# Performance work log

Hardware: AMD Instinct MI355X
Metric: run time of the kernel (lower is better)

## Reference

```python
import jax, jax.numpy as jnp
import numpy as np

C_IN = 128   # pair channel dim
H = 4        # heads
DH = 32      # per-head dim (c_hidden // no_heads = 128 // 4)
R = 96       # low-rank bias rank (hard-coded self.Rank)
N = 384      # sequence length (pair rep is N x N)
S_DIM = 449  # s_inputs feature dim (c_in + 449 into bias MLPs)
MLP_H = 256  # bias MLP hidden width
EPS = 1e-5


def setup_inputs() -> dict:
    key = jax.random.key(0)
    ks = jax.random.split(key, 16)
    w = lambda k, shp, s=0.02: (jax.random.normal(k, shp) * s).astype(jnp.float32)
    return {
        "x": jax.random.normal(ks[0], (N, N, C_IN), dtype=jnp.float32),
        "s_inputs": jax.random.normal(ks[1], (N, S_DIM), dtype=jnp.float32),
        "ln_gamma": jnp.ones((C_IN,), jnp.float32),
        "ln_beta": jnp.zeros((C_IN,), jnp.float32),
        # q flashbias MLP (Linear->Tanh->Linear->Tanh->Linear, no bias)
        "Wq1": w(ks[2], (C_IN + S_DIM, MLP_H)),
        "Wq2": w(ks[3], (MLP_H, MLP_H)),
        "Wq3": w(ks[4], (MLP_H, H * R)),
        # k flashbias MLP
        "Wk1": w(ks[5], (C_IN + S_DIM, MLP_H)),
        "Wk2": w(ks[6], (MLP_H, MLP_H)),
        "Wk3": w(ks[7], (MLP_H, H * R)),
        # OpenFold-style gated Attention params
        "Wq_att": w(ks[8], (C_IN, H * DH)),
        "Wk_att": w(ks[9], (C_IN, H * DH)),
        "Wv_att": w(ks[10], (C_IN, H * DH)),
        "Wg": w(ks[11], (C_IN, H * DH)),
        "bg": jnp.zeros((H * DH,), jnp.float32),
        "Wo": w(ks[12], (H * DH, C_IN)),
        "bo": jnp.zeros((C_IN,), jnp.float32),
        "id": 10,  # id < 16 -> low-rank flashbias path
    }


def _layer_norm(x, gamma, beta):
    mu = jnp.mean(x, axis=-1, keepdims=True)
    var = jnp.var(x, axis=-1, keepdims=True)
    return (x - mu) * jax.lax.rsqrt(var + EPS) * gamma + beta


def _bias_mlp(z, W1, W2, W3):
    # [N, C+449] -> [N, H*R] -> [1, H, N, R]
    h = jnp.tanh(jnp.tanh(z @ W1) @ W2) @ W3
    return jnp.transpose(h.reshape(N, H, R), (1, 0, 2))[None]


def reference(x, s_inputs, ln_gamma, ln_beta, Wq1, Wq2, Wq3, Wk1, Wk2, Wk3,
              Wq_att, Wk_att, Wv_att, Wg, bg, Wo, bo, id=10):
    # starting=True, eval mode, s_inputs given, id < 16 -> low-rank bias path
    x = _layer_norm(x, ln_gamma, ln_beta)                       # [N, N, C]

    # low-rank triangle-bias factors (shared across rows, broadcast over dim 0)
    q_bias = _bias_mlp(jnp.concatenate([x.mean(1), s_inputs], -1), Wq1, Wq2, Wq3)  # [1,H,N,R]
    k_bias = _bias_mlp(jnp.concatenate([x.mean(0), s_inputs], -1), Wk1, Wk2, Wk3)  # [1,H,N,R]

    # multi-head attention over the last sequence axis, per row
    def heads(z, W):  # [N, N, C] -> [N, H, N, DH]
        return jnp.transpose((z @ W).reshape(N, N, H, DH), (0, 2, 1, 3))

    q = heads(x, Wq_att) * (1.0 / np.sqrt(DH)).astype(np.float32)
    k = heads(x, Wk_att)
    v = heads(x, Wv_att)

    scores = jnp.einsum("ihqd,ihkd->ihqk", q, k)                # [N,H,N,N]
    scores = scores + jnp.einsum("bhqr,bhkr->bhqk", q_bias, k_bias)  # broadcast over rows
    a = jax.nn.softmax(scores, axis=-1)

    o = jnp.einsum("ihqk,ihkd->ihqd", a, v)                     # [N,H,N,DH]
    o = jnp.transpose(o, (0, 2, 1, 3)).reshape(N, N, H * DH)
    g = jax.nn.sigmoid(x @ Wg + bg)                              # gating
    out = (g * o) @ Wo + bo                                      # [N, N, C]
    return out
```

## Files before the change

### kernel.cpp

```cpp
#include <hip/hip_runtime.h>
#include <cstdint>
#include <cstddef>

typedef _Float16 f16;
typedef __attribute__((ext_vector_type(2))) _Float16 f16x2;
typedef __attribute__((ext_vector_type(4))) _Float16 f16x4;
typedef __attribute__((ext_vector_type(8))) _Float16 f16x8;
typedef __attribute__((ext_vector_type(4))) float f32x4;

#define MFMA_16x16x32(a,b,c) __builtin_amdgcn_mfma_f32_16x16x32_f16((a),(b),(c),0,0,0)
#define MFMA_16x16x16(a,b,c) __builtin_amdgcn_mfma_f32_16x16x16f16((a),(b),(c),0,0,0)

#define NSEQ 384
#define CIN 128
#define NH 4
#define DHD 32
#define RNK 96
#define SDIM 449
#define MHID 256
#define NN (NSEQ*NSEQ)
#define LOG2E 1.4426950408889634f

#define KPAD 608
#define ZSTR 616
#define HSTR 264
#define OFF_W1 0
#define SZ_W1 (MHID*KPAD)
#define OFF_W2 (2*SZ_W1)
#define SZ_W2 (MHID*MHID)
#define OFF_W3 (OFF_W2 + 2*SZ_W2)
#define SZ_W3 ((NH*RNK)*MHID)
#define WMLP_TOT (OFF_W3 + 2*SZ_W3)

__global__ __launch_bounds__(256) void k_convert(const float* __restrict__ Wq, const float* __restrict__ Wk,
    const float* __restrict__ Wv, const float* __restrict__ Wg, const float* __restrict__ Wo,
    f16* __restrict__ W4T, f16* __restrict__ WoT) {
  int idx = blockIdx.x*256 + threadIdx.x;
  int c = idx >> 7, kk = idx & 127;
  if (c < 512) {
    int mat = c >> 7, cc = c & 127;
    const float* src = mat==0 ? Wq : (mat==1 ? Wk : (mat==2 ? Wv : Wg));
    W4T[c*CIN + kk] = (f16)src[kk*CIN + cc];
  } else {
    int cc = c - 512;
    WoT[cc*CIN + kk] = (f16)Wo[kk*CIN + cc];
  }
}

__global__ __launch_bounds__(256) void k_convert2(const float* __restrict__ Wq1, const float* __restrict__ Wq2,
    const float* __restrict__ Wq3, const float* __restrict__ Wk1, const float* __restrict__ Wk2,
    const float* __restrict__ Wk3, f16* __restrict__ wmlp) {
  int idx = blockIdx.x*256 + threadIdx.x;
  float val;
  if (idx < OFF_W2) {
    int m = idx / SZ_W1, r = idx - m*SZ_W1;
    int c = r / KPAD, kk = r - c*KPAD;
    const float* src = m ? Wk1 : Wq1;
    val = (kk < SDIM + CIN) ? src[kk*MHID + c] : 0.f;
  } else if (idx < OFF_W3) {
    int r = idx - OFF_W2;
    int m = r >> 16, rr = r & 65535;
    int c = rr >> 8, kk = rr & 255;
    const float* src = m ? Wk2 : Wq2;
    val = src[kk*MHID + c];
  } else {
    int r = idx - OFF_W3;
    int m = r / SZ_W3, rr = r - m*SZ_W3;
    int c = rr >> 8, kk = rr & 255;
    const float* src = m ? Wk3 : Wq3;
    val = src[kk*(NH*RNK) + c];
  }
  wmlp[idx] = (f16)val;
}

__global__ __launch_bounds__(256) void k_ln(const float* __restrict__ x, const float* __restrict__ gamma,
    const float* __restrict__ beta, f16* __restrict__ xn, float* __restrict__ rowm) {
  int b = blockIdx.x;
  int i = b >> 2, jbase = (b & 3) * 96;
  int t = threadIdx.x, wave = t >> 6, lane = t & 63;
  int half = lane >> 5, l31 = lane & 31;
  int c0 = l31 * 4;
  __shared__ float racc[CIN];
  if (t < CIN) racc[t] = 0.f;
  float4 g4 = *(const float4*)&gamma[c0];
  float4 b4 = *(const float4*)&beta[c0];
  float a0=0,a1=0,a2=0,a3=0;
  __syncthreads();
  for (int it = 0; it < 12; ++it) {
    int j = jbase + it*8 + wave*2 + half;
    const float4 v = *(const float4*)&x[(size_t)(i*NSEQ + j)*CIN + c0];
    float s = (v.x+v.y)+(v.z+v.w);
    float ss = (v.x*v.x+v.y*v.y)+(v.z*v.z+v.w*v.w);
#pragma unroll
    for (int off = 16; off >= 1; off >>= 1) { s += __shfl_xor(s, off); ss += __shfl_xor(ss, off); }
    float mean = s * (1.0f/CIN);
    float var = ss * (1.0f/CIN) - mean*mean;
    float rs = rsqrtf(var + 1e-5f);
    float y0 = (v.x-mean)*rs*g4.x + b4.x;
    float y1 = (v.y-mean)*rs*g4.y + b4.y;
    float y2 = (v.z-mean)*rs*g4.z + b4.z;
    float y3 = (v.w-mean)*rs*g4.w + b4.w;
    f16x4 w; w[0]=(f16)y0; w[1]=(f16)y1; w[2]=(f16)y2; w[3]=(f16)y3;
    *(f16x4*)&xn[(size_t)(i*NSEQ + j)*CIN + c0] = w;
    a0+=y0; a1+=y1; a2+=y2; a3+=y3;
  }
  atomicAdd(&racc[c0], a0); atomicAdd(&racc[c0+1], a1);
  atomicAdd(&racc[c0+2], a2); atomicAdd(&racc[c0+3], a3);
  __syncthreads();
  if (t < CIN) atomicAdd(&rowm[i*CIN + t], racc[t] * (1.0f/NSEQ));
}

__global__ __launch_bounds__(256) void k_colmean(const f16* __restrict__ xn, float* __restrict__ colm) {
  int j = blockIdx.x; int t = threadIdx.x;
  int c = t & 127, half = t >> 7;
  float acc = 0.f;
  int i0 = half*192;
#pragma unroll 4
  for (int ii = i0; ii < i0 + 192; ++ii)
    acc += (float)xn[(size_t)(ii*NSEQ + j)*CIN + c];
  __shared__ float sb[256];
  sb[t] = acc;
  __syncthreads();
  if (t < 128) colm[j*CIN + t] = (sb[t] + sb[t+128]) * (1.0f/NSEQ);
}

__global__ __launch_bounds__(256) void k_mlp2(const float* __restrict__ rowm, const float* __restrict__ colm,
    const float* __restrict__ sinp, const f16* __restrict__ wmlp,
    float* __restrict__ qbT, float* __restrict__ kbT) {
  int b = blockIdx.x;
  bool isQ = b < 12;
  int r0 = (isQ ? b : b - 12) * 32;
  const float* mean = isQ ? rowm : colm;
  const f16* W1T = wmlp + (isQ ? 0 : SZ_W1);
  const f16* W2T = wmlp + OFF_W2 + (isQ ? 0 : SZ_W2);
  const f16* W3T = wmlp + OFF_W3 + (isQ ? 0 : SZ_W3);
  float* outp = isQ ? qbT : kbT;
  int t = threadIdx.x, wave = t >> 6, lane = t & 63;
  int l15 = lane & 15, quad = lane >> 4;
  int rt = wave & 1, ch = wave >> 1;

  __shared__ __align__(16) f16 z[32*ZSTR];
  __shared__ __align__(16) f16 hbuf[2][32*HSTR];

  for (int idx = t; idx < 32*KPAD; idx += 256) {
    int row = idx / KPAD, u = idx - row*KPAD;
    float v;
    if (u < CIN) v = mean[(r0+row)*CIN + u];
    else if (u < CIN + SDIM) v = sinp[(r0+row)*SDIM + (u - CIN)];
    else v = 0.f;
    z[row*ZSTR + u] = (f16)v;
  }
  __syncthreads();

  {
    f32x4 acc[8];
#pragma unroll
    for (int c = 0; c < 8; ++c) acc[c] = (f32x4){0,0,0,0};
    for (int ks = 0; ks < 19; ++ks) {
      f16x8 af = *(const f16x8*)&z[(rt*16 + l15)*ZSTR + ks*32 + quad*8];
#pragma unroll
      for (int c = 0; c < 8; ++c) {
        f16x8 bf = *(const f16x8*)&W1T[(size_t)((ch*8 + c)*16 + l15)*KPAD + ks*32 + quad*8];
        acc[c] = MFMA_16x16x32(af, bf, acc[c]);
      }
    }
#pragma unroll
    for (int c = 0; c < 8; ++c) {
      int col = (ch*8 + c)*16 + l15;
#pragma unroll
      for (int r = 0; r < 4; ++r) {
        float th = 1.f - 2.f/(1.f + __expf(2.f*acc[c][r]));
        hbuf[0][(rt*16 + quad*4 + r)*HSTR + col] = (f16)th;
      }
    }
  }
  __syncthreads();

  {
    f32x4 acc[8];
#pragma unroll
    for (int c = 0; c < 8; ++c) acc[c] = (f32x4){0,0,0,0};
    for (int ks = 0; ks < 8; ++ks) {
      f16x8 af = *(const f16x8*)&hbuf[0][(rt*16 + l15)*HSTR + ks*32 + quad*8];
#pragma unroll
      for (int c = 0; c < 8; ++c) {
        f16x8 bf = *(const f16x8*)&W2T[(size_t)((ch*8 + c)*16 + l15)*MHID + ks*32 + quad*8];
        acc[c] = MFMA_16x16x32(af, bf, acc[c]);
      }
    }
#pragma unroll
    for (int c = 0; c < 8; ++c) {
      int col = (ch*8 + c)*16 + l15;
#pragma unroll
      for (int r = 0; r < 4; ++r) {
        float th = 1.f - 2.f/(1.f + __expf(2.f*acc[c][r]));
        hbuf[1][(rt*16 + quad*4 + r)*HSTR + col] = (f16)th;
      }
    }
  }
  __syncthreads();

  {
    f32x4 acc[12];
#pragma unroll
    for (int c = 0; c < 12; ++c) acc[c] = (f32x4){0,0,0,0};
    for (int ks = 0; ks < 8; ++ks) {
      f16x8 af = *(const f16x8*)&hbuf[1][(rt*16 + l15)*HSTR + ks*32 + quad*8];
#pragma unroll
      for (int c = 0; c < 12; ++c) {
        f16x8 bf = *(const f16x8*)&W3T[(size_t)((ch*12 + c)*16 + l15)*MHID + ks*32 + quad*8];
        acc[c] = MFMA_16x16x32(af, bf, acc[c]);
      }
    }
#pragma unroll
    for (int c = 0; c < 12; ++c) {
      int o = (ch*12 + c)*16 + l15;
#pragma unroll
      for (int r = 0; r < 4; ++r)
        outp[o*NSEQ + r0 + rt*16 + quad*4 + r] = acc[c][r];
    }
  }
}

__global__ __launch_bounds__(128) void k_bias(const float* __restrict__ qbT, const float* __restrict__ kbT,
    f16* __restrict__ bias4) {
  int b = blockIdx.x;
  int h = b / 96, kg = b - h*96;
  int t = threadIdx.x;
  __shared__ float4 kr[RNK];
  if (t < RNK) kr[t] = *(const float4*)&kbT[(size_t)(h*RNK + t)*NSEQ + kg*4];
  __syncthreads();
  float acc[3][4];
#pragma unroll
  for (int m = 0; m < 3; ++m)
#pragma unroll
    for (int r = 0; r < 4; ++r) acc[m][r] = 0.f;
  for (int r = 0; r < RNK; ++r) {
    float4 kv = kr[r];
    const float* qrow = qbT + (size_t)(h*RNK + r)*NSEQ;
    float q0 = qrow[t], q1 = qrow[t+128], q2 = qrow[t+256];
    acc[0][0]+=q0*kv.x; acc[0][1]+=q0*kv.y; acc[0][2]+=q0*kv.z; acc[0][3]+=q0*kv.w;
    acc[1][0]+=q1*kv.x; acc[1][1]+=q1*kv.y; acc[1][2]+=q1*kv.z; acc[1][3]+=q1*kv.w;
    acc[2][0]+=q2*kv.x; acc[2][1]+=q2*kv.y; acc[2][2]+=q2*kv.z; acc[2][3]+=q2*kv.w;
  }
#pragma unroll
  for (int m = 0; m < 3; ++m) {
    int q = t + m*128;
    f16x4 w; w[0]=(f16)(acc[m][0]*LOG2E); w[1]=(f16)(acc[m][1]*LOG2E);
    w[2]=(f16)(acc[m][2]*LOG2E); w[3]=(f16)(acc[m][3]*LOG2E);
    *(f16x4*)&bias4[((size_t)b*NSEQ + q)*4] = w;
  }
}

__global__ __launch_bounds__(256) void k_proj(const f16* __restrict__ xn, const f16* __restrict__ W4T,
    const float* __restrict__ bg, f16* __restrict__ qb, f16* __restrict__ kb, f16* __restrict__ vb,
    f16* __restrict__ gb) {
  int mb = blockIdx.x;
  int t = threadIdx.x, wave = t >> 6, lane = t & 63;
  int l15 = lane & 15, quad = lane >> 4;
  int m0 = wave*32;
  __shared__ __align__(16) f16 Bs[128*128];
  size_t grow = (size_t)mb*128 + m0;
  f16x8 af[2][4];
#pragma unroll
  for (int mt = 0; mt < 2; ++mt)
#pragma unroll
    for (int kt = 0; kt < 4; ++kt)
      af[mt][kt] = *(const f16x8*)&xn[(grow + mt*16 + l15)*CIN + (kt*4 + quad)*8];
  int i = mb/3, j0 = (mb - (mb/3)*3)*128 + m0;
  for (int nb = 0; nb < 4; ++nb) {
    for (int p = 0; p < 8; ++p) {
      int c = p*256 + t; int row = c >> 4, ci = c & 15;
      int sw = (ci ^ (row & 15)) * 8;
      *(f16x8*)&Bs[row*128 + sw] = *(const f16x8*)&W4T[(size_t)(nb*128 + row)*CIN + ci*8];
    }
    __syncthreads();
#pragma unroll
    for (int ct = 0; ct < 8; ++ct) {
      f32x4 acc0 = (f32x4){0,0,0,0}, acc1 = (f32x4){0,0,0,0};
#pragma unroll
      for (int kt = 0; kt < 4; ++kt) {
        f16x8 bf = *(const f16x8*)&Bs[(ct*16 + l15)*128 + ((kt*4 + quad) ^ l15)*8];
        acc0 = MFMA_16x16x32(af[0][kt], bf, acc0);
        acc1 = MFMA_16x16x32(af[1][kt], bf, acc1);
      }
      int col = nb*128 + ct*16 + l15;
      int cc = col & 127;
      int hh = cc >> 5, d = cc & 31;
      if (nb == 3) {
        float bgv = bg[cc];
#pragma unroll
        for (int mt = 0; mt < 2; ++mt) {
          f32x4 a = mt ? acc1 : acc0;
#pragma unroll
          for (int r = 0; r < 4; ++r) {
            int jj = j0 + mt*16 + quad*4 + r;
            float sg = 1.0f/(1.0f + __expf(-(a[r] + bgv)));
            gb[(size_t)(i*NSEQ + jj)*CIN + cc] = (f16)sg;
          }
        }
      } else {
        f16* dstb = nb==0 ? qb : (nb==1 ? kb : vb);
        float scale = nb==0 ? 0.25503576722f : 1.0f;
#pragma unroll
        for (int mt = 0; mt < 2; ++mt) {
          f32x4 a = mt ? acc1 : acc0;
#pragma unroll
          for (int r = 0; r < 4; ++r) {
            int jj = j0 + mt*16 + quad*4 + r;
            dstb[((size_t)(i*NH + hh)*NSEQ + jj)*DHD + d] = (f16)(a[r]*scale);
          }
        }
      }
    }
    __syncthreads();
  }
}

__global__ __launch_bounds__(256, 4) void k_attn(const f16* __restrict__ qg, const f16* __restrict__ kg,
    const f16* __restrict__ vg, const f16* __restrict__ bias4, f16* __restrict__ og) {
  int b = blockIdx.x; int h = b / NSEQ; int i = b - h*NSEQ;
  int t = threadIdx.x; int wave = t >> 6; int lane = t & 63;
  int l15 = lane & 15, quad = lane >> 4;
  size_t base = (size_t)(i*NH + h) * NSEQ * DHD;
  int qt0 = wave*6;
  f16x8 qf[6];
#pragma unroll
  for (int s = 0; s < 6; ++s)
    qf[s] = *(const f16x8*)&qg[base + (size_t)((qt0+s)*16 + l15)*DHD + quad*8];
  f32x4 oa[6][2];
  float lsum[6];
#pragma unroll
  for (int s = 0; s < 6; ++s) { lsum[s] = 0.f; oa[s][0] = (f32x4){0,0,0,0}; oa[s][1] = (f32x4){0,0,0,0}; }
  const f16* kp = kg + base + (size_t)l15*DHD + quad*8;
  const f16* vp = vg + base + (size_t)(quad*4)*DHD + l15;
  const f16* bp = bias4 + (((size_t)h*96 + quad)*NSEQ + qt0*16 + l15)*4;
  for (int kt = 0; kt < 24; ++kt) {
    f16x8 kf = *(const f16x8*)kp;
    f16x4 vf0, vf1;
#pragma unroll
    for (int jj = 0; jj < 4; ++jj) { vf0[jj] = vp[jj*DHD]; vf1[jj] = vp[jj*DHD + 16]; }
    f32x4 cb[6];
#pragma unroll
    for (int s = 0; s < 6; ++s) {
      f16x4 ch = *(const f16x4*)(bp + s*64);
      cb[s][0] = (float)ch[0]; cb[s][1] = (float)ch[1];
      cb[s][2] = (float)ch[2]; cb[s][3] = (float)ch[3];
    }
    kp += 16*DHD; vp += 16*DHD; bp += 4*NSEQ*4;
#pragma unroll
    for (int s = 0; s < 6; ++s) {
      f32x4 st = MFMA_16x16x32(kf, qf[s], cb[s]);
      float p0 = __builtin_amdgcn_exp2f(st[0]);
      float p1 = __builtin_amdgcn_exp2f(st[1]);
      float p2 = __builtin_amdgcn_exp2f(st[2]);
      float p3 = __builtin_amdgcn_exp2f(st[3]);
      lsum[s] += (p0 + p1) + (p2 + p3);
      f16x4 pa; pa[0]=(f16)p0; pa[1]=(f16)p1; pa[2]=(f16)p2; pa[3]=(f16)p3;
      oa[s][0] = MFMA_16x16x16(pa, vf0, oa[s][0]);
      oa[s][1] = MFMA_16x16x16(pa, vf1, oa[s][1]);
    }
  }
#pragma unroll
  for (int s = 0; s < 6; ++s) {
    float lf = lsum[s];
    lf += __shfl_xor(lf, 16);
    lf += __shfl_xor(lf, 32);
    float inv = 1.0f / lf;
#pragma unroll
    for (int r = 0; r < 4; ++r) {
      float invr = __shfl(inv, quad*4 + r);
      int qrow = (qt0+s)*16 + quad*4 + r;
      size_t ob = (size_t)(i*NSEQ + qrow)*(NH*DHD) + h*DHD;
      og[ob + l15]      = (f16)(oa[s][0][r] * invr);
      og[ob + 16 + l15] = (f16)(oa[s][1][r] * invr);
    }
  }
}

__global__ __launch_bounds__(256) void k_final(const f16* __restrict__ gb, const f16* __restrict__ ob,
    const f16* __restrict__ WoT, const float* __restrict__ bo, float* __restrict__ out) {
  int mb = blockIdx.x;
  int t = threadIdx.x, wave = t >> 6, lane = t & 63;
  int l15 = lane & 15, quad = lane >> 4;
  __shared__ __align__(16) f16 Bs[128*128];
  for (int p = 0; p < 8; ++p) {
    int c = p*256 + t; int row = c >> 4, ci = c & 15;
    int sw = (ci ^ (row & 15)) * 8;
    *(f16x8*)&Bs[row*128 + sw] = *(const f16x8*)&WoT[row*CIN + ci*8];
  }
  int m0 = wave*32;
  size_t grow = (size_t)mb*128 + m0;
  f16x8 af[2][4];
#pragma unroll
  for (int mt = 0; mt < 2; ++mt)
#pragma unroll
    for (int kt = 0; kt < 4; ++kt) {
      size_t off = (grow + mt*16 + l15)*CIN + (kt*4 + quad)*8;
      f16x8 gv = *(const f16x8*)&gb[off];
      f16x8 ov = *(const f16x8*)&ob[off];
      af[mt][kt] = gv*ov;
    }
  __syncthreads();
#pragma unroll
  for (int ct = 0; ct < 8; ++ct) {
    f32x4 acc0 = (f32x4){0,0,0,0}, acc1 = (f32x4){0,0,0,0};
#pragma unroll
    for (int kt = 0; kt < 4; ++kt) {
      f16x8 bf = *(const f16x8*)&Bs[(ct*16 + l15)*128 + ((kt*4 + quad) ^ l15)*8];
      acc0 = MFMA_16x16x32(af[0][kt], bf, acc0);
      acc1 = MFMA_16x16x32(af[1][kt], bf, acc1);
    }
    float bov = bo[ct*16 + l15];
#pragma unroll
    for (int mt = 0; mt < 2; ++mt) {
      f32x4 a = mt ? acc1 : acc0;
#pragma unroll
      for (int r = 0; r < 4; ++r) {
        int mrow = (int)(grow) + mt*16 + quad*4 + r;
        out[(size_t)mrow*CIN + ct*16 + l15] = a[r] + bov;
      }
    }
  }
}

extern "C" void kernel_launch(void* const* d_in, const int* in_sizes, int n_in,
                              void* d_out, int out_size, void* d_ws, size_t ws_size,
                              hipStream_t stream) {
  (void)in_sizes; (void)n_in; (void)out_size; (void)ws_size;
  const float* x    = (const float*)d_in[0];
  const float* sinp = (const float*)d_in[1];
  const float* gam  = (const float*)d_in[2];
  const float* bet  = (const float*)d_in[3];
  const float* Wq1  = (const float*)d_in[4];
  const float* Wq2  = (const float*)d_in[5];
  const float* Wq3  = (const float*)d_in[6];
  const float* Wk1  = (const float*)d_in[7];
  const float* Wk2  = (const float*)d_in[8];
  const float* Wk3  = (const float*)d_in[9];
  const float* Wqa  = (const float*)d_in[10];
  const float* Wka  = (const float*)d_in[11];
  const float* Wva  = (const float*)d_in[12];
  const float* Wg   = (const float*)d_in[13];
  const float* bg   = (const float*)d_in[14];
  const float* Wo   = (const float*)d_in[15];
  const float* bo   = (const float*)d_in[16];
  float* out = (float*)d_out;

  char* w = (char*)d_ws;
  auto carve = [&](size_t bytes) { char* p = w; w += (bytes + 255) & ~(size_t)255; return p; };
  f16*   xn    = (f16*)carve((size_t)NN*CIN*2);
  f16*   qb    = (f16*)carve((size_t)NN*CIN*2);
  f16*   kb    = (f16*)carve((size_t)NN*CIN*2);
  f16*   vb    = (f16*)carve((size_t)NN*CIN*2);
  f16*   gbuf  = (f16*)carve((size_t)NN*CIN*2);
  f16*   bias4 = (f16*)carve((size_t)NH*NSEQ*NSEQ*2);
  float* rowm  = (float*)carve((size_t)NSEQ*CIN*4);
  float* colm  = (float*)carve((size_t)NSEQ*CIN*4);
  float* qbT   = (float*)carve((size_t)(NH*RNK)*NSEQ*4);
  float* kbT   = (float*)carve((size_t)(NH*RNK)*NSEQ*4);
  f16*   W4T   = (f16*)carve((size_t)512*CIN*2);
  f16*   WoT   = (f16*)carve((size_t)CIN*CIN*2);
  f16*   wmlp  = (f16*)carve((size_t)WMLP_TOT*2);
  f16*   obuf  = xn;

  hipMemsetAsync(rowm, 0, (size_t)NSEQ*CIN*4, stream);
  k_convert<<<320, 256, 0, stream>>>(Wqa, Wka, Wva, Wg, Wo, W4T, WoT);
  k_convert2<<<WMLP_TOT/256, 256, 0, stream>>>(Wq1, Wq2, Wq3, Wk1, Wk2, Wk3, wmlp);
  k_ln<<<NSEQ*4, 256, 0, stream>>>(x, gam, bet, xn, rowm);
  k_colmean<<<NSEQ, 256, 0, stream>>>(xn, colm);
  k_mlp2<<<24, 256, 0, stream>>>(rowm, colm, sinp, wmlp, qbT, kbT);
  k_bias<<<NH*96, 128, 0, stream>>>(qbT, kbT, bias4);
  k_proj<<<1152, 256, 0, stream>>>(xn, W4T, bg, qb, kb, vb, gbuf);
  k_attn<<<NH*NSEQ, 256, 0, stream>>>(qb, kb, vb, bias4, obuf);
  k_final<<<1152, 256, 0, stream>>>(gbuf, obuf, WoT, bo, out);
}
```

Baseline: 450.4 us.

## Stage fp32 attention bias through double-buffered LDS via direct global-to-LDS loads

The low-rank bias is now stored in fp32 instead of fp16. The attention kernel streams each key tile's bias into a two-slot LDS buffer using global_load_lds, prefetching the next tile while the current one is consumed. This replaces per-lane strided global loads and fp16-to-fp32 conversions with LDS reads. In exchange it doubles bias memory traffic, adds a __syncthreads every key tile, uses 48KB of LDS per block, and drops the occupancy hint in launch_bounds, all of which can lower occupancy.

```diff
diff --git a/kernel.cpp b/kernel.cpp
--- a/kernel.cpp
+++ b/kernel.cpp
@@ -31,6 +31,10 @@
 #define OFF_W3 (OFF_W2 + 2*SZ_W2)
 #define SZ_W3 ((NH*RNK)*MHID)
 #define WMLP_TOT (OFF_W3 + 2*SZ_W3)
+
+#define GLOAD_LDS16(g, l) __builtin_amdgcn_global_load_lds( \
+    (const __attribute__((address_space(1))) void*)(g), \
+    (__attribute__((address_space(3))) void*)(l), 16, 0, 0)
 
 __global__ __launch_bounds__(256) void k_convert(const float* __restrict__ Wq, const float* __restrict__ Wk,
     const float* __restrict__ Wv, const float* __restrict__ Wg, const float* __restrict__ Wo,
@@ -223,7 +227,7 @@
 }
 
 __global__ __launch_bounds__(128) void k_bias(const float* __restrict__ qbT, const float* __restrict__ kbT,
-    f16* __restrict__ bias4) {
+    float* __restrict__ bias4) {
   int b = blockIdx.x;
   int h = b / 96, kg = b - h*96;
   int t = threadIdx.x;
@@ -246,9 +250,8 @@
 #pragma unroll
   for (int m = 0; m < 3; ++m) {
     int q = t + m*128;
-    f16x4 w; w[0]=(f16)(acc[m][0]*LOG2E); w[1]=(f16)(acc[m][1]*LOG2E);
-    w[2]=(f16)(acc[m][2]*LOG2E); w[3]=(f16)(acc[m][3]*LOG2E);
-    *(f16x4*)&bias4[((size_t)b*NSEQ + q)*4] = w;
+    f32x4 w; w[0]=acc[m][0]*LOG2E; w[1]=acc[m][1]*LOG2E; w[2]=acc[m][2]*LOG2E; w[3]=acc[m][3]*LOG2E;
+    *(f32x4*)&bias4[((size_t)b*NSEQ + q)*4] = w;
   }
 }
 
@@ -317,13 +320,14 @@
   }
 }
 
-__global__ __launch_bounds__(256, 4) void k_attn(const f16* __restrict__ qg, const f16* __restrict__ kg,
-    const f16* __restrict__ vg, const f16* __restrict__ bias4, f16* __restrict__ og) {
+__global__ __launch_bounds__(256) void k_attn(const f16* __restrict__ qg, const f16* __restrict__ kg,
+    const f16* __restrict__ vg, const float* __restrict__ bias4, f16* __restrict__ og) {
   int b = blockIdx.x; int h = b / NSEQ; int i = b - h*NSEQ;
   int t = threadIdx.x; int wave = t >> 6; int lane = t & 63;
   int l15 = lane & 15, quad = lane >> 4;
   size_t base = (size_t)(i*NH + h) * NSEQ * DHD;
   int qt0 = wave*6;
+  __shared__ __align__(16) float lbias[2][6144];
   f16x8 qf[6];
 #pragma unroll
   for (int s = 0; s < 6; ++s)
@@ -334,20 +338,31 @@
   for (int s = 0; s < 6; ++s) { lsum[s] = 0.f; oa[s][0] = (f32x4){0,0,0,0}; oa[s][1] = (f32x4){0,0,0,0}; }
   const f16* kp = kg + base + (size_t)l15*DHD + quad*8;
   const f16* vp = vg + base + (size_t)(quad*4)*DHD + l15;
-  const f16* bp = bias4 + (((size_t)h*96 + quad)*NSEQ + qt0*16 + l15)*4;
+  const char* gb0 = (const char*)(bias4 + (size_t)h*96*NSEQ*4);
+  int stoff = wave*6144 + lane*16;
+#pragma unroll
+  for (int u = 0; u < 6; ++u)
+    GLOAD_LDS16(gb0 + stoff + u*1024, (char*)&lbias[0][0] + wave*6144 + u*1024);
+  const float* lrd0 = &lbias[0][quad*1536 + (qt0*16 + l15)*4];
+  const float* lrd1 = &lbias[1][quad*1536 + (qt0*16 + l15)*4];
   for (int kt = 0; kt < 24; ++kt) {
+    __syncthreads();
     f16x8 kf = *(const f16x8*)kp;
     f16x4 vf0, vf1;
 #pragma unroll
     for (int jj = 0; jj < 4; ++jj) { vf0[jj] = vp[jj*DHD]; vf1[jj] = vp[jj*DHD + 16]; }
+    kp += 16*DHD; vp += 16*DHD;
+    if (kt < 23) {
+      const char* src = gb0 + (size_t)(kt+1)*24576;
+      char* ldst = (char*)&lbias[(kt+1)&1][0];
+#pragma unroll
+      for (int u = 0; u < 6; ++u)
+        GLOAD_LDS16(src + stoff + u*1024, ldst + wave*6144 + u*1024);
+    }
+    const float* lr = (kt & 1) ? lrd1 : lrd0;
     f32x4 cb[6];
 #pragma unroll
-    for (int s = 0; s < 6; ++s) {
-      f16x4 ch = *(const f16x4*)(bp + s*64);
-      cb[s][0] = (float)ch[0]; cb[s][1] = (float)ch[1];
-      cb[s][2] = (float)ch[2]; cb[s][3] = (float)ch[3];
-    }
-    kp += 16*DHD; vp += 16*DHD; bp += 4*NSEQ*4;
+    for (int s = 0; s < 6; ++s) cb[s] = *(const f32x4*)(lr + s*64);
 #pragma unroll
     for (int s = 0; s < 6; ++s) {
       f32x4 st = MFMA_16x16x32(kf, qf[s], cb[s]);
@@ -454,7 +469,7 @@
   f16*   kb    = (f16*)carve((size_t)NN*CIN*2);
   f16*   vb    = (f16*)carve((size_t)NN*CIN*2);
   f16*   gbuf  = (f16*)carve((size_t)NN*CIN*2);
-  f16*   bias4 = (f16*)carve((size_t)NH*NSEQ*NSEQ*2);
+  float* bias4 = (float*)carve((size_t)NH*NSEQ*NSEQ*4);
   float* rowm  = (float*)carve((size_t)NSEQ*CIN*4);
   float* colm  = (float*)carve((size_t)NSEQ*CIN*4);
   float* qbT   = (float*)carve((size_t)(NH*RNK)*NSEQ*4);
```

Result: no change. 457.5 us (+1.6%).
